# Kernel tuning notes

Measured on AMD Instinct MI355X. Metric: run time of the kernel, lower is better.

## Reference

```python
import jax, jax.numpy as jnp
import numpy as np


def setup_inputs() -> dict:
    key = jax.random.key(0)
    ks = jax.random.split(key, 9)
    N, C, SY, SX = 256, 128, 11, 25
    DM, DC, D = 64, 64, 128
    return {
        "f_t_global": jax.random.normal(ks[0], (N, D), dtype=jnp.float32),
        "x_t_local": jax.random.normal(ks[1], (N, C, SY, SX), dtype=jnp.float32),
        "x_t_prev_local": jax.random.normal(ks[2], (N, C, SY, SX), dtype=jnp.float32),
        "m_t": jax.random.normal(ks[3], (N, DM), dtype=jnp.float32),
        "m_t_prev": jax.random.normal(ks[4], (N, DM), dtype=jnp.float32),
        "c_t": jax.random.normal(ks[5], (N, DC), dtype=jnp.float32),
        "c_t_prev": jax.random.normal(ks[6], (N, DC), dtype=jnp.float32),
        "W_join": jax.random.normal(ks[7], (C + DM + DC, D), dtype=jnp.float32) * 0.05,
        "b_join": jax.random.normal(ks[8], (D,), dtype=jnp.float32) * 0.05,
    }


def reference(f_t_global, x_t_local, x_t_prev_local, m_t, m_t_prev, c_t, c_t_prev, W_join, b_join):
    N, C, SY, SX = x_t_local.shape
    P = SY * SX
    DM = m_t.shape[1]
    # join_obs(local, m, c) = concat([local, m, c]) @ W_join + b_join, split for efficiency
    Wl = W_join[:C]                 # [C, D]
    Wm = W_join[C:C + DM]           # [DM, D]
    Wc = W_join[C + DM:]            # [DC, D]
    # [N, C, SY, SX] -> [P, N, C]: all spatial positions batched at once
    loc_t = x_t_local.reshape(N, C, P).transpose(2, 0, 1)
    loc_p = x_t_prev_local.reshape(N, C, P).transpose(2, 0, 1)
    bias_t = m_t @ Wm + c_t @ Wc + b_join             # [N, D], shared across positions
    bias_p = m_t_prev @ Wm + c_t_prev @ Wc + b_join   # [N, D]
    positive = jnp.einsum('pnc,cd->pnd', loc_p, Wl) + bias_p[None]  # [P, N, D]
    pred_loc = jnp.einsum('pnc,cd->pnd', loc_t, Wl) + bias_t[None]  # [P, N, D]

    # loss1: global prediction vs per-position prev-local positives
    logits1 = jnp.einsum('nd,pmd->pnm', f_t_global, positive)   # [P, N, N]
    # loss2: per-position current-local vs per-position prev-local
    logits2 = jnp.einsum('pnd,pmd->pnm', pred_loc, positive)    # [P, N, N]

    def mean_infonce(logits):
        # cross_entropy(logits, arange(N)) averaged over batch, then over positions
        lse = jax.nn.logsumexp(logits, axis=-1)            # [P, N]
        diag = jnp.diagonal(logits, axis1=1, axis2=2)      # [P, N]
        return jnp.mean(lse - diag)

    loss1 = mean_infonce(logits1)
    loss2 = mean_infonce(logits2)
    return loss1 + loss2
```

## Files before the change

kernel.cpp:

```cpp
#include <hip/hip_runtime.h>

#define Nn 256
#define Cc 128
#define Pp 275
#define Dd 128

typedef unsigned int u32;
typedef unsigned short u16;
typedef float f32x4 __attribute__((ext_vector_type(4)));
typedef short bf16x8 __attribute__((ext_vector_type(8)));

__device__ __forceinline__ float bf2f(u16 h) {
    return __uint_as_float(((u32)h) << 16);
}
__device__ __forceinline__ u16 f2bf(float f) {
    u32 u = __float_as_uint(f);
    return (u16)((u + 0x7fffu + ((u >> 16) & 1u)) >> 16);
}

__global__ __launch_bounds__(256) void bias_kernel(
    const float* __restrict__ m_t, const float* __restrict__ m_p,
    const float* __restrict__ c_t, const float* __restrict__ c_p,
    const float* __restrict__ W, const float* __restrict__ b,
    const float* __restrict__ f,
    float* __restrict__ bias_t, float* __restrict__ bias_p,
    u16* __restrict__ f_bf, u16* __restrict__ WlT)
{
    int idx = blockIdx.x * 256 + threadIdx.x;
    int n = idx >> 7, d = idx & 127;
    float at = 0.f, ap = 0.f;
#pragma unroll 8
    for (int k = 0; k < 64; ++k) {
        float wm = W[(128 + k) * 128 + d];
        float wc = W[(192 + k) * 128 + d];
        at = fmaf(m_t[n * 64 + k], wm, at);
        at = fmaf(c_t[n * 64 + k], wc, at);
        ap = fmaf(m_p[n * 64 + k], wm, ap);
        ap = fmaf(c_p[n * 64 + k], wc, ap);
    }
    float bb = b[d];
    bias_t[idx] = at + bb;
    bias_p[idx] = ap + bb;
    f_bf[idx] = f2bf(f[idx]);
    if (idx < 16384) {
        int dd = idx >> 7, cc = idx & 127;
        WlT[idx] = f2bf(W[cc * 128 + dd]);
    }
}

__global__ __launch_bounds__(256) void join_direct_kernel(
    const float* __restrict__ x_t, const float* __restrict__ x_p,
    const u16* __restrict__ WlT,
    const float* __restrict__ bias_t, const float* __restrict__ bias_p,
    u16* __restrict__ pred, u16* __restrict__ pos)
{
    __shared__ u16 lds[128 * 128];
    const int tid = threadIdx.x;
    const int n = blockIdx.y;
    const int w = tid >> 6;
    const int l = tid & 63;

    {
        const uint4* src = reinterpret_cast<const uint4*>(WlT);
#pragma unroll
        for (int it = 0; it < 8; ++it) {
            int j = tid + 256 * it;
            int row = j >> 4;
            int colb = (j & 15) << 4;
            uint4 v = src[j];
            *reinterpret_cast<uint4*>((char*)lds + row * 256 + (colb ^ ((row & 7) << 4))) = v;
        }
    }

    const int t = blockIdx.x * 4 + w;
    __syncthreads();
    if (t >= 18) return;

    const int p0 = t * 16;
    int prow = p0 + (l & 15);
    if (prow > Pp - 1) prow = Pp - 1;

    const float* xs_t = x_t + (size_t)n * (Cc * Pp) + prow;
    const float* xs_p = x_p + (size_t)n * (Cc * Pp) + prow;

    bf16x8 At[4], Ap[4];
#pragma unroll
    for (int kk = 0; kk < 4; ++kk) {
        const int c0 = kk * 32 + ((l >> 4) << 3);
        float vt[8], vp[8];
#pragma unroll
        for (int e = 0; e < 8; ++e) vt[e] = xs_t[(size_t)(c0 + e) * Pp];
#pragma unroll
        for (int e = 0; e < 8; ++e) vp[e] = xs_p[(size_t)(c0 + e) * Pp];
        bf16x8 a, c;
#pragma unroll
        for (int e = 0; e < 8; ++e) { a[e] = (short)f2bf(vt[e]); c[e] = (short)f2bf(vp[e]); }
        At[kk] = a;
        Ap[kk] = c;
    }

    float bvT[8], bvP[8];
#pragma unroll
    for (int dt = 0; dt < 8; ++dt) {
        int d = dt * 16 + (l & 15);
        bvT[dt] = bias_t[n * 128 + d];
        bvP[dt] = bias_p[n * 128 + d];
    }

#pragma unroll
    for (int dt = 0; dt < 8; ++dt) {
        bf16x8 B[4];
        const int row = dt * 16 + (l & 15);
#pragma unroll
        for (int kk = 0; kk < 4; ++kk) {
            int cbyte = kk * 64 + ((l >> 4) << 4);
            B[kk] = *reinterpret_cast<const bf16x8*>(
                (const char*)lds + row * 256 + (cbyte ^ ((row & 7) << 4)));
        }
        f32x4 aT = {0.f, 0.f, 0.f, 0.f}, aP = {0.f, 0.f, 0.f, 0.f};
#pragma unroll
        for (int kk = 0; kk < 4; ++kk) {
            aT = __builtin_amdgcn_mfma_f32_16x16x32_bf16(At[kk], B[kk], aT, 0, 0, 0);
            aP = __builtin_amdgcn_mfma_f32_16x16x32_bf16(Ap[kk], B[kk], aP, 0, 0, 0);
        }
        const int d = dt * 16 + (l & 15);
#pragma unroll
        for (int r = 0; r < 4; ++r) {
            int p = p0 + ((l >> 4) << 2) + r;
            if (p < Pp) {
                size_t o = ((size_t)p * Nn + n) * Dd + d;
                pred[o] = f2bf(aT[r] + bvT[dt]);
                pos[o]  = f2bf(aP[r] + bvP[dt]);
            }
        }
    }
}

__global__ __launch_bounds__(512) void logits_mfma_kernel(
    const u16* __restrict__ f_bf,
    const u16* __restrict__ pred, const u16* __restrict__ pos,
    float* __restrict__ partial)
{
    __shared__ u16 lds[Nn * Dd];
    const int tid = threadIdx.x;
    const int p = blockIdx.x;
    const int sel = blockIdx.y;
    const int w = tid >> 6;
    const int l = tid & 63;
    const int r0 = w * 32;

    {
        const uint4* src = reinterpret_cast<const uint4*>(pos + (size_t)p * (Nn * Dd));
#pragma unroll
        for (int it = 0; it < 8; ++it) {
            int j = tid + 512 * it;
            int row = j >> 4;
            int colb = (j & 15) << 4;
            uint4 v = src[j];
            *reinterpret_cast<uint4*>((char*)lds + row * 256 + (colb ^ ((row & 7) << 4))) = v;
        }
    }

    const u16* Abase = sel ? (pred + (size_t)p * (Nn * Dd)) : f_bf;
    bf16x8 A[2][4];
    {
        const int arow = l & 15;
        const int acol = (l >> 4) << 4;
#pragma unroll
        for (int rt = 0; rt < 2; ++rt)
#pragma unroll
            for (int kk = 0; kk < 4; ++kk) {
                const char* ap = (const char*)Abase
                               + (size_t)(r0 + rt * 16 + arow) * 256 + kk * 64 + acol;
                A[rt][kk] = *reinterpret_cast<const bf16x8*>(ap);
            }
    }

    __syncthreads();

    const float L2E = 1.4426950408889634f;
    float s_[2][4];
    float dg[2][4];
#pragma unroll
    for (int rt = 0; rt < 2; ++rt)
#pragma unroll
        for (int r = 0; r < 4; ++r) { s_[rt][r] = 0.f; dg[rt][r] = 0.f; }

    const int mcol = l & 15;
    const int bcol = (l >> 4) << 4;

    for (int ct = 0; ct < 16; ++ct) {
        bf16x8 B[4];
        const int mrow = ct * 16 + mcol;
#pragma unroll
        for (int kk = 0; kk < 4; ++kk) {
            int cb = kk * 64 + bcol;
            B[kk] = *reinterpret_cast<const bf16x8*>(
                (const char*)lds + mrow * 256 + (cb ^ ((mrow & 7) << 4)));
        }
#pragma unroll
        for (int rt = 0; rt < 2; ++rt) {
            f32x4 acc = {0.f, 0.f, 0.f, 0.f};
#pragma unroll
            for (int kk = 0; kk < 4; ++kk)
                acc = __builtin_amdgcn_mfma_f32_16x16x32_bf16(A[rt][kk], B[kk], acc, 0, 0, 0);
            const bool isdg_ct = (ct == ((r0 >> 4) + rt));
#pragma unroll
            for (int r = 0; r < 4; ++r) {
                float v = acc[r];
                s_[rt][r] += __builtin_amdgcn_exp2f(fmaf(v, L2E, -64.f));
                if (isdg_ct && ((l & 15) == (((l >> 4) << 2) + r))) dg[rt][r] = v;
            }
        }
    }

    float local = 0.f;
#pragma unroll
    for (int rt = 0; rt < 2; ++rt)
#pragma unroll
        for (int r = 0; r < 4; ++r) {
            float s = s_[rt][r];
            s += __shfl_xor(s, 1);
            s += __shfl_xor(s, 2);
            s += __shfl_xor(s, 4);
            s += __shfl_xor(s, 8);
            if ((l & 15) == (((l >> 4) << 2) + r))
                local += 0.6931471805599453f * (64.f + __log2f(s)) - dg[rt][r];
        }

    __syncthreads();
    float* red = reinterpret_cast<float*>(lds);
    red[tid] = local;
    __syncthreads();
    for (int k = 256; k > 0; k >>= 1) {
        if (tid < k) red[tid] += red[tid + k];
        __syncthreads();
    }
    if (tid == 0) partial[p * 2 + sel] = red[0];
}

__global__ __launch_bounds__(256) void reduce_kernel(
    const float* __restrict__ partial, float* __restrict__ out)
{
    __shared__ float red[256];
    float s = 0.f;
    for (int i = threadIdx.x; i < 2 * Pp; i += 256) s += partial[i];
    red[threadIdx.x] = s;
    __syncthreads();
    for (int k = 128; k > 0; k >>= 1) {
        if (threadIdx.x < k) red[threadIdx.x] += red[threadIdx.x + k];
        __syncthreads();
    }
    if (threadIdx.x == 0) out[0] = red[0] * (1.0f / (Pp * (float)Nn));
}

extern "C" void kernel_launch(void* const* d_in, const int* in_sizes, int n_in,
                              void* d_out, int out_size, void* d_ws, size_t ws_size,
                              hipStream_t stream)
{
    const float* f   = (const float*)d_in[0];
    const float* x_t = (const float*)d_in[1];
    const float* x_p = (const float*)d_in[2];
    const float* m_t = (const float*)d_in[3];
    const float* m_p = (const float*)d_in[4];
    const float* c_t = (const float*)d_in[5];
    const float* c_p = (const float*)d_in[6];
    const float* W   = (const float*)d_in[7];
    const float* b   = (const float*)d_in[8];

    char* ws = (char*)d_ws;
    const size_t SLAB = (size_t)Pp * Nn * Dd;

    float* bias_t = (float*)ws;
    float* bias_p = bias_t + Nn * Dd;
    u16* f_bf = (u16*)(ws + 262144);
    u16* WlT  = f_bf + Nn * Dd;
    u16* pred = (u16*)(ws + 360448);
    u16* pos  = pred + SLAB;
    float* partial = (float*)(pos + SLAB);

    bias_kernel<<<dim3(Nn * Dd / 256), 256, 0, stream>>>(m_t, m_p, c_t, c_p, W, b, f,
                                                         bias_t, bias_p, f_bf, WlT);
    join_direct_kernel<<<dim3(5, Nn), 256, 0, stream>>>(x_t, x_p, WlT, bias_t, bias_p,
                                                        pred, pos);
    logits_mfma_kernel<<<dim3(Pp, 2), 512, 0, stream>>>(f_bf, pred, pos, partial);
    reduce_kernel<<<1, 256, 0, stream>>>(partial, (float*)d_out);
}
```

Measured before the change: 75.01 us.

## Merge both logits passes into one block sharing pos LDS; hoist x loads before sync

The logits kernel now launches one 1024-thread block per position, where even waves compute loss1 and odd waves compute loss2. The positive slab is loaded into LDS once instead of twice, which halves the LDS fill traffic for pos. In the join kernel, the global loads of the local features are issued before the barrier so they overlap with staging the weights into LDS, and the kernel gets a launch_bounds occupancy hint. Risks are higher register pressure from the 64 held floats and fewer, larger blocks, which can hurt scheduling.

```diff
diff --git a/kernel.cpp b/kernel.cpp
--- a/kernel.cpp
+++ b/kernel.cpp
@@ -48,7 +48,7 @@
     }
 }
 
-__global__ __launch_bounds__(256) void join_direct_kernel(
+__global__ __launch_bounds__(256, 2) void join_direct_kernel(
     const float* __restrict__ x_t, const float* __restrict__ x_p,
     const u16* __restrict__ WlT,
     const float* __restrict__ bias_t, const float* __restrict__ bias_p,
@@ -73,28 +73,41 @@
     }
 
     const int t = blockIdx.x * 4 + w;
+
+    float vt[32], vp[32];
+    {
+        int prow = t * 16 + (l & 15);
+        if (prow > Pp - 1) prow = Pp - 1;
+        const float* xs_t = x_t + (size_t)n * (Cc * Pp) + prow;
+        const float* xs_p = x_p + (size_t)n * (Cc * Pp) + prow;
+        const int cg = (l >> 4) << 3;
+#pragma unroll
+        for (int kk = 0; kk < 4; ++kk) {
+            const size_t cb = (size_t)(kk * 32 + cg) * Pp;
+#pragma unroll
+            for (int e = 0; e < 8; ++e) vt[kk * 8 + e] = xs_t[cb + (size_t)e * Pp];
+        }
+#pragma unroll
+        for (int kk = 0; kk < 4; ++kk) {
+            const size_t cb = (size_t)(kk * 32 + cg) * Pp;
+#pragma unroll
+            for (int e = 0; e < 8; ++e) vp[kk * 8 + e] = xs_p[cb + (size_t)e * Pp];
+        }
+    }
+
     __syncthreads();
     if (t >= 18) return;
-
     const int p0 = t * 16;
-    int prow = p0 + (l & 15);
-    if (prow > Pp - 1) prow = Pp - 1;
-
-    const float* xs_t = x_t + (size_t)n * (Cc * Pp) + prow;
-    const float* xs_p = x_p + (size_t)n * (Cc * Pp) + prow;
 
     bf16x8 At[4], Ap[4];
 #pragma unroll
     for (int kk = 0; kk < 4; ++kk) {
-        const int c0 = kk * 32 + ((l >> 4) << 3);
-        float vt[8], vp[8];
-#pragma unroll
-        for (int e = 0; e < 8; ++e) vt[e] = xs_t[(size_t)(c0 + e) * Pp];
-#pragma unroll
-        for (int e = 0; e < 8; ++e) vp[e] = xs_p[(size_t)(c0 + e) * Pp];
         bf16x8 a, c;
 #pragma unroll
-        for (int e = 0; e < 8; ++e) { a[e] = (short)f2bf(vt[e]); c[e] = (short)f2bf(vp[e]); }
+        for (int e = 0; e < 8; ++e) {
+            a[e] = (short)f2bf(vt[kk * 8 + e]);
+            c[e] = (short)f2bf(vp[kk * 8 + e]);
+        }
         At[kk] = a;
         Ap[kk] = c;
     }
@@ -136,7 +149,7 @@
     }
 }
 
-__global__ __launch_bounds__(512) void logits_mfma_kernel(
+__global__ __launch_bounds__(1024) void logits_mfma_kernel(
     const u16* __restrict__ f_bf,
     const u16* __restrict__ pred, const u16* __restrict__ pos,
     float* __restrict__ partial)
@@ -144,16 +157,16 @@
     __shared__ u16 lds[Nn * Dd];
     const int tid = threadIdx.x;
     const int p = blockIdx.x;
-    const int sel = blockIdx.y;
     const int w = tid >> 6;
     const int l = tid & 63;
-    const int r0 = w * 32;
+    const int sel = w & 1;
+    const int r0 = (w >> 1) * 32;
 
     {
         const uint4* src = reinterpret_cast<const uint4*>(pos + (size_t)p * (Nn * Dd));
 #pragma unroll
-        for (int it = 0; it < 8; ++it) {
-            int j = tid + 512 * it;
+        for (int it = 0; it < 4; ++it) {
+            int j = tid + 1024 * it;
             int row = j >> 4;
             int colb = (j & 15) << 4;
             uint4 v = src[j];
@@ -232,11 +245,11 @@
     float* red = reinterpret_cast<float*>(lds);
     red[tid] = local;
     __syncthreads();
-    for (int k = 256; k > 0; k >>= 1) {
+    for (int k = 512; k > 0; k >>= 1) {
         if (tid < k) red[tid] += red[tid + k];
         __syncthreads();
     }
-    if (tid == 0) partial[p * 2 + sel] = red[0];
+    if (tid == 0) partial[p] = red[0];
 }
 
 __global__ __launch_bounds__(256) void reduce_kernel(
@@ -244,7 +257,7 @@
 {
     __shared__ float red[256];
     float s = 0.f;
-    for (int i = threadIdx.x; i < 2 * Pp; i += 256) s += partial[i];
+    for (int i = threadIdx.x; i < Pp; i += 256) s += partial[i];
     red[threadIdx.x] = s;
     __syncthreads();
     for (int k = 128; k > 0; k >>= 1) {
@@ -283,6 +296,6 @@
                                                          bias_t, bias_p, f_bf, WlT);
     join_direct_kernel<<<dim3(5, Nn), 256, 0, stream>>>(x_t, x_p, WlT, bias_t, bias_p,
                                                         pred, pos);
-    logits_mfma_kernel<<<dim3(Pp, 2), 512, 0, stream>>>(f_bf, pred, pos, partial);
+    logits_mfma_kernel<<<dim3(Pp), 1024, 0, stream>>>(f_bf, pred, pos, partial);
     reduce_kernel<<<1, 256, 0, stream>>>(partial, (float*)d_out);
 }
```

After: 82.14 us. 9.5% more time.

## Drop LDS staging of projection weights and split join kernel by input tensor

Applied to the files above, without the earlier changes.

The join kernel no longer stages the 32KB transposed weight matrix into shared memory with a block-wide barrier. Each wave now reads its B fragments directly from global memory, where they should hit in L2/L1. A third grid dimension splits the current and previous inputs into separate blocks, doubling the block count and halving per-thread register usage. The trade-off is repeated global/cache loads of the weights instead of LDS reads, and wasted blocks where whole waves exit early.

```diff
diff --git a/kernel.cpp b/kernel.cpp
--- a/kernel.cpp
+++ b/kernel.cpp
@@ -48,90 +48,70 @@
     }
 }
 
-__global__ __launch_bounds__(256) void join_direct_kernel(
+__global__ __launch_bounds__(256) void join_nolds_kernel(
     const float* __restrict__ x_t, const float* __restrict__ x_p,
     const u16* __restrict__ WlT,
     const float* __restrict__ bias_t, const float* __restrict__ bias_p,
     u16* __restrict__ pred, u16* __restrict__ pos)
 {
-    __shared__ u16 lds[128 * 128];
     const int tid = threadIdx.x;
     const int n = blockIdx.y;
+    const int pass = blockIdx.z;
     const int w = tid >> 6;
     const int l = tid & 63;
-
-    {
-        const uint4* src = reinterpret_cast<const uint4*>(WlT);
-#pragma unroll
-        for (int it = 0; it < 8; ++it) {
-            int j = tid + 256 * it;
-            int row = j >> 4;
-            int colb = (j & 15) << 4;
-            uint4 v = src[j];
-            *reinterpret_cast<uint4*>((char*)lds + row * 256 + (colb ^ ((row & 7) << 4))) = v;
-        }
-    }
-
     const int t = blockIdx.x * 4 + w;
-    __syncthreads();
     if (t >= 18) return;
+
+    const float* xg  = pass ? x_p : x_t;
+    const float* bias = pass ? bias_p : bias_t;
+    u16* outp = pass ? pos : pred;
 
     const int p0 = t * 16;
     int prow = p0 + (l & 15);
     if (prow > Pp - 1) prow = Pp - 1;
 
-    const float* xs_t = x_t + (size_t)n * (Cc * Pp) + prow;
-    const float* xs_p = x_p + (size_t)n * (Cc * Pp) + prow;
-
-    bf16x8 At[4], Ap[4];
+    const float* xs = xg + (size_t)n * (Cc * Pp) + prow;
+    const int cg = (l >> 4) << 3;
+
+    float v[32];
 #pragma unroll
     for (int kk = 0; kk < 4; ++kk) {
-        const int c0 = kk * 32 + ((l >> 4) << 3);
-        float vt[8], vp[8];
-#pragma unroll
-        for (int e = 0; e < 8; ++e) vt[e] = xs_t[(size_t)(c0 + e) * Pp];
-#pragma unroll
-        for (int e = 0; e < 8; ++e) vp[e] = xs_p[(size_t)(c0 + e) * Pp];
-        bf16x8 a, c;
-#pragma unroll
-        for (int e = 0; e < 8; ++e) { a[e] = (short)f2bf(vt[e]); c[e] = (short)f2bf(vp[e]); }
-        At[kk] = a;
-        Ap[kk] = c;
-    }
-
-    float bvT[8], bvP[8];
-#pragma unroll
-    for (int dt = 0; dt < 8; ++dt) {
-        int d = dt * 16 + (l & 15);
-        bvT[dt] = bias_t[n * 128 + d];
-        bvP[dt] = bias_p[n * 128 + d];
-    }
+        const size_t cb = (size_t)(kk * 32 + cg) * Pp;
+#pragma unroll
+        for (int e = 0; e < 8; ++e) v[kk * 8 + e] = xs[cb + (size_t)e * Pp];
+    }
+    asm volatile("" ::: "memory");
+
+    bf16x8 A[4];
+#pragma unroll
+    for (int kk = 0; kk < 4; ++kk) {
+        bf16x8 a;
+#pragma unroll
+        for (int e = 0; e < 8; ++e) a[e] = (short)f2bf(v[kk * 8 + e]);
+        A[kk] = a;
+    }
+
+    float bv[8];
+#pragma unroll
+    for (int dt = 0; dt < 8; ++dt) bv[dt] = bias[n * 128 + dt * 16 + (l & 15)];
+
+    const char* Bbase = (const char*)WlT + ((l & 15) << 8) + ((l >> 4) << 4);
 
 #pragma unroll
     for (int dt = 0; dt < 8; ++dt) {
         bf16x8 B[4];
-        const int row = dt * 16 + (l & 15);
-#pragma unroll
-        for (int kk = 0; kk < 4; ++kk) {
-            int cbyte = kk * 64 + ((l >> 4) << 4);
-            B[kk] = *reinterpret_cast<const bf16x8*>(
-                (const char*)lds + row * 256 + (cbyte ^ ((row & 7) << 4)));
-        }
-        f32x4 aT = {0.f, 0.f, 0.f, 0.f}, aP = {0.f, 0.f, 0.f, 0.f};
-#pragma unroll
-        for (int kk = 0; kk < 4; ++kk) {
-            aT = __builtin_amdgcn_mfma_f32_16x16x32_bf16(At[kk], B[kk], aT, 0, 0, 0);
-            aP = __builtin_amdgcn_mfma_f32_16x16x32_bf16(Ap[kk], B[kk], aP, 0, 0, 0);
-        }
+#pragma unroll
+        for (int kk = 0; kk < 4; ++kk)
+            B[kk] = *reinterpret_cast<const bf16x8*>(Bbase + dt * 4096 + kk * 64);
+        f32x4 acc = {0.f, 0.f, 0.f, 0.f};
+#pragma unroll
+        for (int kk = 0; kk < 4; ++kk)
+            acc = __builtin_amdgcn_mfma_f32_16x16x32_bf16(A[kk], B[kk], acc, 0, 0, 0);
         const int d = dt * 16 + (l & 15);
 #pragma unroll
         for (int r = 0; r < 4; ++r) {
             int p = p0 + ((l >> 4) << 2) + r;
-            if (p < Pp) {
-                size_t o = ((size_t)p * Nn + n) * Dd + d;
-                pred[o] = f2bf(aT[r] + bvT[dt]);
-                pos[o]  = f2bf(aP[r] + bvP[dt]);
-            }
+            if (p < Pp) outp[((size_t)p * Nn + n) * Dd + d] = f2bf(acc[r] + bv[dt]);
         }
     }
 }
@@ -281,8 +261,8 @@
 
     bias_kernel<<<dim3(Nn * Dd / 256), 256, 0, stream>>>(m_t, m_p, c_t, c_p, W, b, f,
                                                          bias_t, bias_p, f_bf, WlT);
-    join_direct_kernel<<<dim3(5, Nn), 256, 0, stream>>>(x_t, x_p, WlT, bias_t, bias_p,
-                                                        pred, pos);
+    join_nolds_kernel<<<dim3(5, Nn, 2), 256, 0, stream>>>(x_t, x_p, WlT, bias_t, bias_p,
+                                                          pred, pos);
     logits_mfma_kernel<<<dim3(Pp, 2), 512, 0, stream>>>(f_bf, pred, pos, partial);
     reduce_kernel<<<1, 256, 0, stream>>>(partial, (float*)d_out);
 }
```

Result: slower. 91.34 us (+21.8%).

## Stage local features through LDS with vectorized loads and reorder logits grid

Applied to the files above, without the earlier changes.

The join kernel now cooperatively loads each block's 32-position by 128-channel tile of both local inputs with 16-byte loads, converts it to bf16, and writes it into swizzled LDS. MFMA A fragments are then read from LDS, replacing the earlier per-lane strided scalar global loads. The work is split across 9 position chunks, with each wave covering 16 positions and half of the D tiles. This makes the dominant input read more coalesced, but more blocks now reload the weight tile into LDS per batch row. The logits grid is also swapped so that both selections for the same position are scheduled next to each other, which should improve L2 reuse of the shared positive slab.

```diff
diff --git a/kernel.cpp b/kernel.cpp
--- a/kernel.cpp
+++ b/kernel.cpp
@@ -48,17 +48,19 @@
     }
 }
 
-__global__ __launch_bounds__(256) void join_direct_kernel(
+__global__ __launch_bounds__(256) void join_stage_kernel(
     const float* __restrict__ x_t, const float* __restrict__ x_p,
     const u16* __restrict__ WlT,
     const float* __restrict__ bias_t, const float* __restrict__ bias_p,
     u16* __restrict__ pred, u16* __restrict__ pos)
 {
-    __shared__ u16 lds[128 * 128];
+    __shared__ u16 wlds[128 * 128];
+    __shared__ u16 xt_lds[32 * 128];
+    __shared__ u16 xp_lds[32 * 128];
     const int tid = threadIdx.x;
+    const int chunk = blockIdx.x;
     const int n = blockIdx.y;
-    const int w = tid >> 6;
-    const int l = tid & 63;
+    const int p0 = chunk * 32;
 
     {
         const uint4* src = reinterpret_cast<const uint4*>(WlT);
@@ -68,54 +70,84 @@
             int row = j >> 4;
             int colb = (j & 15) << 4;
             uint4 v = src[j];
-            *reinterpret_cast<uint4*>((char*)lds + row * 256 + (colb ^ ((row & 7) << 4))) = v;
-        }
-    }
-
-    const int t = blockIdx.x * 4 + w;
-    __syncthreads();
-    if (t >= 18) return;
-
-    const int p0 = t * 16;
-    int prow = p0 + (l & 15);
-    if (prow > Pp - 1) prow = Pp - 1;
-
-    const float* xs_t = x_t + (size_t)n * (Cc * Pp) + prow;
-    const float* xs_p = x_p + (size_t)n * (Cc * Pp) + prow;
+            *reinterpret_cast<uint4*>((char*)wlds + row * 256 + (colb ^ ((row & 7) << 4))) = v;
+        }
+    }
+
+    {
+        const float* xbt = x_t + (size_t)n * (Cc * Pp);
+        const float* xbp = x_p + (size_t)n * (Cc * Pp);
+        const int p4 = tid & 7;
+        const int prow = p0 + p4 * 4;
+        const bool full = (prow + 3 < Pp);
+#pragma unroll
+        for (int j = 0; j < 2; ++j) {
+            const int c0 = (tid >> 3) * 2 + 64 * j;
+            float a0[4], a1[4], b0[4], b1[4];
+            if (full) {
+                f32x4 t0 = *reinterpret_cast<const f32x4*>(xbt + (size_t)c0 * Pp + prow);
+                f32x4 t1 = *reinterpret_cast<const f32x4*>(xbt + (size_t)(c0 + 1) * Pp + prow);
+                f32x4 q0 = *reinterpret_cast<const f32x4*>(xbp + (size_t)c0 * Pp + prow);
+                f32x4 q1 = *reinterpret_cast<const f32x4*>(xbp + (size_t)(c0 + 1) * Pp + prow);
+#pragma unroll
+                for (int e = 0; e < 4; ++e) { a0[e]=t0[e]; a1[e]=t1[e]; b0[e]=q0[e]; b1[e]=q1[e]; }
+            } else {
+#pragma unroll
+                for (int e = 0; e < 4; ++e) {
+                    int pe = prow + e; if (pe > Pp - 1) pe = Pp - 1;
+                    a0[e] = xbt[(size_t)c0 * Pp + pe];
+                    a1[e] = xbt[(size_t)(c0 + 1) * Pp + pe];
+                    b0[e] = xbp[(size_t)c0 * Pp + pe];
+                    b1[e] = xbp[(size_t)(c0 + 1) * Pp + pe];
+                }
+            }
+#pragma unroll
+            for (int e = 0; e < 4; ++e) {
+                const int pl = p4 * 4 + e;
+                const int cb = (c0 * 2) ^ ((pl & 7) << 4);
+                *reinterpret_cast<u32*>((char*)xt_lds + pl * 256 + cb) =
+                    (u32)f2bf(a0[e]) | ((u32)f2bf(a1[e]) << 16);
+                *reinterpret_cast<u32*>((char*)xp_lds + pl * 256 + cb) =
+                    (u32)f2bf(b0[e]) | ((u32)f2bf(b1[e]) << 16);
+            }
+        }
+    }
+
+    __syncthreads();
+
+    const int w = tid >> 6;
+    const int l = tid & 63;
+    const int tw = w >> 1;
+    const int dt0 = (w & 1) * 4;
+    const int g = l >> 4;
+    const int pl_in = tw * 16 + (l & 15);
 
     bf16x8 At[4], Ap[4];
 #pragma unroll
     for (int kk = 0; kk < 4; ++kk) {
-        const int c0 = kk * 32 + ((l >> 4) << 3);
-        float vt[8], vp[8];
-#pragma unroll
-        for (int e = 0; e < 8; ++e) vt[e] = xs_t[(size_t)(c0 + e) * Pp];
-#pragma unroll
-        for (int e = 0; e < 8; ++e) vp[e] = xs_p[(size_t)(c0 + e) * Pp];
-        bf16x8 a, c;
-#pragma unroll
-        for (int e = 0; e < 8; ++e) { a[e] = (short)f2bf(vt[e]); c[e] = (short)f2bf(vp[e]); }
-        At[kk] = a;
-        Ap[kk] = c;
-    }
-
-    float bvT[8], bvP[8];
-#pragma unroll
-    for (int dt = 0; dt < 8; ++dt) {
-        int d = dt * 16 + (l & 15);
-        bvT[dt] = bias_t[n * 128 + d];
-        bvP[dt] = bias_p[n * 128 + d];
-    }
-
-#pragma unroll
-    for (int dt = 0; dt < 8; ++dt) {
+        const int cb = (kk * 64 + g * 16) ^ ((pl_in & 7) << 4);
+        At[kk] = *reinterpret_cast<const bf16x8*>((const char*)xt_lds + pl_in * 256 + cb);
+        Ap[kk] = *reinterpret_cast<const bf16x8*>((const char*)xp_lds + pl_in * 256 + cb);
+    }
+
+    float bvT[4], bvP[4];
+#pragma unroll
+    for (int i = 0; i < 4; ++i) {
+        int d = (dt0 + i) * 16 + (l & 15);
+        bvT[i] = bias_t[n * 128 + d];
+        bvP[i] = bias_p[n * 128 + d];
+    }
+
+#pragma unroll
+    for (int i = 0; i < 4; ++i) {
+        const int dt = dt0 + i;
         bf16x8 B[4];
         const int row = dt * 16 + (l & 15);
 #pragma unroll
         for (int kk = 0; kk < 4; ++kk) {
-            int cbyte = kk * 64 + ((l >> 4) << 4);
+            int cbyte = kk * 64 + (g << 4);
             B[kk] = *reinterpret_cast<const bf16x8*>(
-                (const char*)lds + row * 256 + (cbyte ^ ((row & 7) << 4)));
+                (const char*)wlds + row * 256 + (cbyte ^ ((row & 7) << 4)));
         }
         f32x4 aT = {0.f, 0.f, 0.f, 0.f}, aP = {0.f, 0.f, 0.f, 0.f};
 #pragma unroll
@@ -126,11 +158,11 @@
         const int d = dt * 16 + (l & 15);
 #pragma unroll
         for (int r = 0; r < 4; ++r) {
-            int p = p0 + ((l >> 4) << 2) + r;
+            int p = p0 + tw * 16 + g * 4 + r;
             if (p < Pp) {
                 size_t o = ((size_t)p * Nn + n) * Dd + d;
-                pred[o] = f2bf(aT[r] + bvT[dt]);
-                pos[o]  = f2bf(aP[r] + bvP[dt]);
+                pred[o] = f2bf(aT[r] + bvT[i]);
+                pos[o]  = f2bf(aP[r] + bvP[i]);
             }
         }
     }
@@ -143,8 +175,8 @@
 {
     __shared__ u16 lds[Nn * Dd];
     const int tid = threadIdx.x;
-    const int p = blockIdx.x;
-    const int sel = blockIdx.y;
+    const int sel = blockIdx.x;
+    const int p = blockIdx.y;
     const int w = tid >> 6;
     const int l = tid & 63;
     const int r0 = w * 32;
@@ -281,8 +313,8 @@
 
     bias_kernel<<<dim3(Nn * Dd / 256), 256, 0, stream>>>(m_t, m_p, c_t, c_p, W, b, f,
                                                          bias_t, bias_p, f_bf, WlT);
-    join_direct_kernel<<<dim3(5, Nn), 256, 0, stream>>>(x_t, x_p, WlT, bias_t, bias_p,
-                                                        pred, pos);
-    logits_mfma_kernel<<<dim3(Pp, 2), 512, 0, stream>>>(f_bf, pred, pos, partial);
+    join_stage_kernel<<<dim3(9, Nn), 256, 0, stream>>>(x_t, x_p, WlT, bias_t, bias_p,
+                                                       pred, pos);
+    logits_mfma_kernel<<<dim3(2, Pp), 512, 0, stream>>>(f_bf, pred, pos, partial);
     reduce_kernel<<<1, 256, 0, stream>>>(partial, (float*)d_out);
 }
```

Measured after the change: 76.36 us. No clear change (+1.8%).
